# Kernel tuning notes

Measured on AMD Instinct MI355X. Metric: run time of the kernel, lower is better.

## Reference

```python
import jax, jax.numpy as jnp
from jax import lax
import numpy as np

# sym6 reconstruction low-pass (pywt Wavelet('sym6').filter_bank[2]), length 12
SYM6_REC = [-0.007800708325034148, 0.0017677118642428036, 0.04472490177066578,
            -0.021060292512300564, -0.07263752278646252, 0.3379294217276218,
            0.787641141030194, 0.4910559419267466, -0.048311742585633,
            -0.11799011114819057, 0.0034907120842174702, 0.015404109327027373]

UP, DOWN = 1, 2
PAD = (len(SYM6_REC) - UP) // 2  # = 5


def setup_inputs() -> dict:
    key = jax.random.key(0)
    h = jnp.asarray(SYM6_REC, dtype=jnp.float32)
    kernel = h[None, :] * h[:, None]  # [12, 12] separable outer product
    x = jax.random.normal(key, (16, 64, 256, 256), dtype=jnp.float32)
    return {"input": x, "kernel": kernel}


def reference(input, kernel):
    # upfirdn2d: zero-insert upsample (lhs_dilation), pad, FIR convolve
    # (true convolution => flip kernel for lax correlation), strided downsample.
    B, C, H, W = input.shape
    w = jnp.flip(kernel, (0, 1))[None, None]        # [1, 1, kh, kw]
    x = input.reshape(B * C, 1, H, W)               # depthwise via batch fold
    y = lax.conv_general_dilated(
        x, w,
        window_strides=(DOWN, DOWN),
        padding=[(PAD, PAD), (PAD, PAD)],
        lhs_dilation=(UP, UP),
        dimension_numbers=('NCHW', 'OIHW', 'NCHW'))
    return y.reshape(B, C, y.shape[-2], y.shape[-1])
```

## Files before the change

kernel.cpp:

```cpp
#include <hip/hip_runtime.h>


#define H_IN  256
#define W_IN  256
#define H_OUT 128
#define W_OUT 128
#define KTAP  12
#define TOR   64
#define VSTR  148
#define NTHR  192

typedef float f32x4 __attribute__((ext_vector_type(4)));

__global__ __launch_bounds__(NTHR)
void upfirdn2d_sym6(const float* __restrict__ x,
                    const float* __restrict__ k2d,
                    float* __restrict__ out) {
    __shared__ float vs[TOR * VSTR];
    __shared__ float ks[KTAP * KTAP];
    __shared__ float wsh[KTAP];

    const int tid = threadIdx.x;

    if (tid < KTAP * KTAP) ks[tid] = k2d[tid];
    __syncthreads();
    if (tid < KTAP) {
        float tot = 0.f;
        #pragma unroll
        for (int i = 0; i < KTAP * KTAP; ++i) tot += ks[i];
        float rs = 0.f;
        #pragma unroll
        for (int q = 0; q < KTAP; ++q) rs += ks[(KTAP - 1 - tid) * KTAP + q];
        wsh[tid] = rs * rsqrtf(tot);
    }
    __syncthreads();
    float w[KTAP];
    #pragma unroll
    for (int p = 0; p < KTAP; ++p) w[p] = wsh[p];

    const int img = blockIdx.y;
    const int ti  = blockIdx.x >> 1;
    const int tj  = blockIdx.x & 1;
    const float* xim = x + (size_t)img * (H_IN * W_IN);
    float* oim = out + (size_t)img * (H_OUT * W_OUT);

    const int gc0 = 128 * tj - 8;

    if (tid < 144) {
        const int rg  = tid / 36;
        const int cg  = tid - rg * 36;
        const int col = gc0 + 4 * cg;
        const bool colok = (unsigned)col < (unsigned)W_IN;
        const int i0  = rg * 16;
        const int gr0 = 2 * (64 * ti + i0) - 5;

        float4 acc[16];
        #pragma unroll
        for (int k = 0; k < 16; ++k) acc[k] = make_float4(0.f, 0.f, 0.f, 0.f);

        const float* rp = xim + (size_t)gr0 * W_IN + col;
        #pragma unroll
        for (int rr = 0; rr < 42; ++rr) {
            const int gr = gr0 + rr;
            float4 v = make_float4(0.f, 0.f, 0.f, 0.f);
            if (colok && (unsigned)gr < (unsigned)H_IN)
                v = *reinterpret_cast<const float4*>(rp);
            rp += W_IN;
            #pragma unroll
            for (int ri = 0; ri < 16; ++ri) {
                const int p = rr - 2 * ri;
                if (p >= 0 && p < KTAP) {
                    acc[ri].x = fmaf(w[p], v.x, acc[ri].x);
                    acc[ri].y = fmaf(w[p], v.y, acc[ri].y);
                    acc[ri].z = fmaf(w[p], v.z, acc[ri].z);
                    acc[ri].w = fmaf(w[p], v.w, acc[ri].w);
                }
            }
        }
        #pragma unroll
        for (int ri = 0; ri < 16; ++ri)
            *reinterpret_cast<float4*>(&vs[(i0 + ri) * VSTR + 4 * cg]) = acc[ri];
    }
    __syncthreads();

    for (int t = tid; t < 512; t += NTHR) {
        const int i = t >> 3;
        const int g = t & 7;

        float f[32];
        #pragma unroll
        for (int m = 0; m < 8; ++m) {
            float4 v4 = *reinterpret_cast<const float4*>(&vs[i * VSTR + 16 * g + 4 * m]);
            f[4*m+0] = v4.x; f[4*m+1] = v4.y; f[4*m+2] = v4.z; f[4*m+3] = v4.w;
        }
        float o[8];
        #pragma unroll
        for (int jj = 0; jj < 8; ++jj) {
            float a = 0.f;
            #pragma unroll
            for (int q = 0; q < KTAP; ++q)
                a = fmaf(w[q], f[2*jj + 3 + q], a);
            o[jj] = a;
        }
        const int orow = 64 * ti + i;
        const int ocol = 64 * tj + 8 * g;
        f32x4 o0 = { o[0], o[1], o[2], o[3] };
        f32x4 o1 = { o[4], o[5], o[6], o[7] };
        float* dst = oim + (size_t)orow * W_OUT + ocol;
        __builtin_nontemporal_store(o0, reinterpret_cast<f32x4*>(dst));
        __builtin_nontemporal_store(o1, reinterpret_cast<f32x4*>(dst + 4));
    }
}

extern "C" void kernel_launch(void* const* d_in, const int* in_sizes, int n_in,
                              void* d_out, int out_size, void* d_ws, size_t ws_size,
                              hipStream_t stream) {
    const float* x   = (const float*)d_in[0];
    const float* k2d = (const float*)d_in[1];
    float* out       = (float*)d_out;

    dim3 grid(4, 1024);
    dim3 block(NTHR);
    upfirdn2d_sym6<<<grid, block, 0, stream>>>(x, k2d, out);
}
```

Baseline: 70.88 us.

## Retile to full-width 32-row strips with swizzled 1D grid and simpler weight setup

Each block now covers a full-width strip of 32 output rows instead of a 64x64 quadrant. This removes the horizontal halo columns that neighbouring tiles loaded twice, and the vertical pass uses 136 of 256 threads. The grid becomes 1D with a block-index swizzle that spreads consecutive blocks across image groups. The weight setup reads kernel rows with vector loads and drops one barrier and the shared 2D kernel copy. In exchange, the vertical halo rows are re-read more often relative to output, and more threads sit idle during the vertical pass.

Result: faster. 62.90 us (-11.3%).

```diff
diff --git a/kernel.cpp b/kernel.cpp
--- a/kernel.cpp
+++ b/kernel.cpp
@@ -6,9 +6,9 @@
 #define H_OUT 128
 #define W_OUT 128
 #define KTAP  12
-#define TOR   64
-#define VSTR  148
-#define NTHR  192
+#define VSTR  276
+#define FG    68
+#define NTHR  256
 
 typedef float f32x4 __attribute__((ext_vector_type(4)));
 
@@ -16,43 +16,44 @@
 void upfirdn2d_sym6(const float* __restrict__ x,
                     const float* __restrict__ k2d,
                     float* __restrict__ out) {
-    __shared__ float vs[TOR * VSTR];
-    __shared__ float ks[KTAP * KTAP];
-    __shared__ float wsh[KTAP];
+    __shared__ float vs[32 * VSTR];
+    __shared__ float rsum[KTAP];
 
     const int tid = threadIdx.x;
 
-    if (tid < KTAP * KTAP) ks[tid] = k2d[tid];
-    __syncthreads();
     if (tid < KTAP) {
-        float tot = 0.f;
-        #pragma unroll
-        for (int i = 0; i < KTAP * KTAP; ++i) tot += ks[i];
-        float rs = 0.f;
-        #pragma unroll
-        for (int q = 0; q < KTAP; ++q) rs += ks[(KTAP - 1 - tid) * KTAP + q];
-        wsh[tid] = rs * rsqrtf(tot);
+        const float4* kp = reinterpret_cast<const float4*>(k2d + 12 * tid);
+        float4 a = kp[0], b = kp[1], c = kp[2];
+        rsum[tid] = ((a.x + a.y) + (a.z + a.w))
+                  + ((b.x + b.y) + (b.z + b.w))
+                  + ((c.x + c.y) + (c.z + c.w));
     }
     __syncthreads();
     float w[KTAP];
-    #pragma unroll
-    for (int p = 0; p < KTAP; ++p) w[p] = wsh[p];
+    {
+        float tot = 0.f;
+        #pragma unroll
+        for (int q = 0; q < KTAP; ++q) tot += rsum[q];
+        const float r = rsqrtf(tot);
+        #pragma unroll
+        for (int p = 0; p < KTAP; ++p) w[p] = rsum[KTAP - 1 - p] * r;
+    }
 
-    const int img = blockIdx.y;
-    const int ti  = blockIdx.x >> 1;
-    const int tj  = blockIdx.x & 1;
+    const int bid = blockIdx.x;
+    const int nb  = (bid & 7) * 512 + (bid >> 3);
+    const int img = nb >> 2;
+    const int ti  = nb & 3;
+
     const float* xim = x + (size_t)img * (H_IN * W_IN);
     float* oim = out + (size_t)img * (H_OUT * W_OUT);
 
-    const int gc0 = 128 * tj - 8;
-
-    if (tid < 144) {
-        const int rg  = tid / 36;
-        const int cg  = tid - rg * 36;
-        const int col = gc0 + 4 * cg;
+    if (tid < 136) {
+        const int rg  = tid / FG;
+        const int cg  = tid - rg * FG;
+        const int col = -8 + 4 * cg;
         const bool colok = (unsigned)col < (unsigned)W_IN;
-        const int i0  = rg * 16;
-        const int gr0 = 2 * (64 * ti + i0) - 5;
+        const int i0  = 16 * rg;
+        const int gr0 = 64 * ti + 32 * rg - 5;
 
         float4 acc[16];
         #pragma unroll
@@ -84,8 +85,8 @@
     __syncthreads();
 
     for (int t = tid; t < 512; t += NTHR) {
-        const int i = t >> 3;
-        const int g = t & 7;
+        const int i = t >> 4;
+        const int g = t & 15;
 
         float f[32];
         #pragma unroll
@@ -102,8 +103,8 @@
                 a = fmaf(w[q], f[2*jj + 3 + q], a);
             o[jj] = a;
         }
-        const int orow = 64 * ti + i;
-        const int ocol = 64 * tj + 8 * g;
+        const int orow = 32 * ti + i;
+        const int ocol = 8 * g;
         f32x4 o0 = { o[0], o[1], o[2], o[3] };
         f32x4 o1 = { o[4], o[5], o[6], o[7] };
         float* dst = oim + (size_t)orow * W_OUT + ocol;
@@ -119,7 +120,7 @@
     const float* k2d = (const float*)d_in[1];
     float* out       = (float*)d_out;
 
-    dim3 grid(4, 1024);
+    dim3 grid(4096);
     dim3 block(NTHR);
     upfirdn2d_sym6<<<grid, block, 0, stream>>>(x, k2d, out);
 }
```
